# Optimization experiments

Hardware: AMD Instinct MI355X
Metric: run time of the kernel (lower is better)

## Reference

```python
import jax, jax.numpy as jnp
import numpy as np

SEQ_LEN = 512
JOINT_DIM = 96
DECAY = 0.8


def _predefined_weights(n: int, decay: float) -> np.ndarray:
    # W[i, j] = decay**(i-j) for j <= i, each row normalized to sum 1.
    i = np.arange(n)[:, None]
    j = np.arange(n)[None, :]
    lower = j <= i
    exponent = np.where(lower, i - j, 0)
    w = np.where(lower, decay ** exponent.astype(np.float64), 0.0)
    row_sum = w.sum(axis=1, keepdims=True)
    w = np.where(row_sum > 0, w / row_sum, w)
    return w.astype(np.float32)


def setup_inputs() -> dict:
    key = jax.random.key(0)
    kx, ko = jax.random.split(key)
    x = jax.random.normal(kx, (64, SEQ_LEN, JOINT_DIM), dtype=jnp.float32)
    # learnable parameter (initialized to zeros in the module; small noise for generality)
    learnable_offset = 0.02 * jax.random.normal(ko, (JOINT_DIM, SEQ_LEN, SEQ_LEN), dtype=jnp.float32)
    predefined_weights = jnp.asarray(_predefined_weights(SEQ_LEN, DECAY))
    return {"x": x, "learnable_offset": learnable_offset, "predefined_weights": predefined_weights}


def reference(x, learnable_offset, predefined_weights):
    # masks[j] = softmax(predefined + offset[j], axis=-1)   -> [J, N, N]
    masks = jax.nn.softmax(predefined_weights[None, :, :] + learnable_offset, axis=-1)
    # out[b, n, j] = sum_m masks[j, n, m] * x[b, m, j]      -> [B, N, J]
    return jnp.einsum('jnm,bmj->bnj', masks, x)
```

## Files before the change

### kernel.cpp

```cpp
#include <hip/hip_runtime.h>

#define BATCH 64
#define SEQ   512
#define JDIM  96
#define TN    64
#define KC    64
#define NCH   (SEQ / KC)
#define LDB   72

typedef __attribute__((ext_vector_type(8))) short bf16x8;
typedef __attribute__((ext_vector_type(4))) float f32x4;

__device__ __forceinline__ unsigned short f2bf(float f) {
  unsigned u = __float_as_uint(f);
  u += 0x7FFFu + ((u >> 16) & 1u);
  return (unsigned short)(u >> 16);
}

__global__ __launch_bounds__(256) void transpose_in_kernel(
    const float* __restrict__ x, unsigned short* __restrict__ xT) {
  __shared__ float tile[JDIM * 65];
  const int r0 = blockIdx.x * 64;
  const int R = BATCH * SEQ;
  for (int idx = threadIdx.x; idx < 64 * 24; idx += 256) {
    int rr = idx / 24, jg = idx - rr * 24;
    float4 v = *(const float4*)(x + (size_t)(r0 + rr) * JDIM + 4 * jg);
    tile[(4 * jg + 0) * 65 + rr] = v.x;
    tile[(4 * jg + 1) * 65 + rr] = v.y;
    tile[(4 * jg + 2) * 65 + rr] = v.z;
    tile[(4 * jg + 3) * 65 + rr] = v.w;
  }
  __syncthreads();
  for (int idx = threadIdx.x; idx < JDIM * 8; idx += 256) {
    int jj = idx >> 3, rg = idx & 7;
    const float* t = &tile[jj * 65 + 8 * rg];
    uint4 pk;
    pk.x = (unsigned)f2bf(t[0]) | ((unsigned)f2bf(t[1]) << 16);
    pk.y = (unsigned)f2bf(t[2]) | ((unsigned)f2bf(t[3]) << 16);
    pk.z = (unsigned)f2bf(t[4]) | ((unsigned)f2bf(t[5]) << 16);
    pk.w = (unsigned)f2bf(t[6]) | ((unsigned)f2bf(t[7]) << 16);
    *(uint4*)(&xT[(size_t)jj * R + r0 + 8 * rg]) = pk;
  }
}

__global__ __launch_bounds__(256, 3) void fused_kernel(
    const unsigned short* __restrict__ xT,
    const float* __restrict__ off,
    const float* __restrict__ pre,
    float* __restrict__ outT) {
  __shared__ unsigned short As[BATCH * LDB];
  __shared__ unsigned short Bs[TN * LDB];
  __shared__ float Lred[TN * 17];
  __shared__ float Linv[TN];

  const int j  = blockIdx.x % JDIM;
  const int n0 = (blockIdx.x / JDIM) * TN;

  const int tid  = threadIdx.x;
  const int lane = tid & 63;
  const int wid  = tid >> 6;
  const int ln   = lane & 15;
  const int quad = lane >> 4;
  const int bw   = (wid & 1) * 32;
  const int nw   = (wid >> 1) * 32;

  f32x4 acc[2][2];
#pragma unroll
  for (int i = 0; i < 2; ++i)
#pragma unroll
    for (int q = 0; q < 2; ++q) acc[i][q] = (f32x4){0.f, 0.f, 0.f, 0.f};
  float Lpart[4] = {0.f, 0.f, 0.f, 0.f};

  const unsigned short* xTj = xT + (size_t)j * (BATCH * SEQ);
  const float* offj = off + (size_t)j * (SEQ * SEQ);

  const int a_kg = tid & 7;
  const int a_b  = tid >> 3;
  const int b_mg = tid & 15;
  const int b_n  = tid >> 4;

  const unsigned short* pA = xTj + (size_t)a_b * SEQ + 8 * a_kg;
  const float* pO = offj + (size_t)(n0 + b_n) * SEQ + 4 * b_mg;
  const float* pP = pre  + (size_t)(n0 + b_n) * SEQ + 4 * b_mg;

  uint4  rA[2];
  float4 rO[4], rP[4];

  rA[0] = *(const uint4*)(pA);
  rA[1] = *(const uint4*)(pA + 32 * SEQ);
#pragma unroll
  for (int p = 0; p < 4; ++p) {
    rO[p] = *(const float4*)(pO + (size_t)(16 * p) * SEQ);
    rP[p] = *(const float4*)(pP + (size_t)(16 * p) * SEQ);
  }

  for (int ch = 0; ch < NCH; ++ch) {
    *(uint4*)(&As[a_b * LDB + 8 * a_kg]) = rA[0];
    *(uint4*)(&As[(a_b + 32) * LDB + 8 * a_kg]) = rA[1];
#pragma unroll
    for (int p = 0; p < 4; ++p) {
      const float e0 = __expf(rO[p].x + rP[p].x);
      const float e1 = __expf(rO[p].y + rP[p].y);
      const float e2 = __expf(rO[p].z + rP[p].z);
      const float e3 = __expf(rO[p].w + rP[p].w);
      Lpart[p] += (e0 + e1) + (e2 + e3);
      uint2 pk;
      pk.x = (unsigned)f2bf(e0) | ((unsigned)f2bf(e1) << 16);
      pk.y = (unsigned)f2bf(e2) | ((unsigned)f2bf(e3) << 16);
      *(uint2*)(&Bs[(b_n + 16 * p) * LDB + 4 * b_mg]) = pk;
    }
    __syncthreads();

    if (ch + 1 < NCH) {
      const int m1 = (ch + 1) * KC;
      rA[0] = *(const uint4*)(pA + m1);
      rA[1] = *(const uint4*)(pA + 32 * SEQ + m1);
#pragma unroll
      for (int p = 0; p < 4; ++p) {
        rO[p] = *(const float4*)(pO + (size_t)(16 * p) * SEQ + m1);
        rP[p] = *(const float4*)(pP + (size_t)(16 * p) * SEQ + m1);
      }
    }

#pragma unroll
    for (int ks = 0; ks < KC; ks += 32) {
      bf16x8 afrag[2], bfrag[2];
#pragma unroll
      for (int i = 0; i < 2; ++i)
        afrag[i] = *(const bf16x8*)(&As[(bw + 16 * i + ln) * LDB + ks + 8 * quad]);
#pragma unroll
      for (int q = 0; q < 2; ++q)
        bfrag[q] = *(const bf16x8*)(&Bs[(nw + 16 * q + ln) * LDB + ks + 8 * quad]);
#pragma unroll
      for (int i = 0; i < 2; ++i)
#pragma unroll
        for (int q = 0; q < 2; ++q)
          acc[i][q] = __builtin_amdgcn_mfma_f32_16x16x32_bf16(afrag[i], bfrag[q], acc[i][q], 0, 0, 0);
    }
    __syncthreads();
  }

#pragma unroll
  for (int p = 0; p < 4; ++p) Lred[(b_n + 16 * p) * 17 + b_mg] = Lpart[p];
  __syncthreads();
  if (tid < TN) {
    float s = 0.f;
#pragma unroll
    for (int i = 0; i < 16; ++i) s += Lred[tid * 17 + i];
    Linv[tid] = 1.0f / s;
  }
  __syncthreads();

  float* outTj = outT + (size_t)j * (SEQ * BATCH);
#pragma unroll
  for (int q = 0; q < 2; ++q) {
    const int nc = nw + 16 * q + ln;
    const float linv = Linv[nc];
#pragma unroll
    for (int i = 0; i < 2; ++i) {
      float4 v;
      v.x = acc[i][q][0] * linv;
      v.y = acc[i][q][1] * linv;
      v.z = acc[i][q][2] * linv;
      v.w = acc[i][q][3] * linv;
      *(float4*)(&outTj[(size_t)(n0 + nc) * BATCH + bw + 16 * i + 4 * quad]) = v;
    }
  }
}

__global__ __launch_bounds__(256) void transpose_out_kernel(
    const float* __restrict__ outT, float* __restrict__ out) {
  __shared__ float tile[JDIM * 65];
  const int n = blockIdx.x;
  for (int idx = threadIdx.x; idx < JDIM * 16; idx += 256) {
    int jj = idx >> 4, g = idx & 15;
    float4 v = *(const float4*)(outT + ((size_t)jj * SEQ + n) * BATCH + 4 * g);
    float* t = &tile[jj * 65 + 4 * g];
    t[0] = v.x; t[1] = v.y; t[2] = v.z; t[3] = v.w;
  }
  __syncthreads();
  for (int idx = threadIdx.x; idx < BATCH * 24; idx += 256) {
    int b = idx / 24, jg = idx - b * 24;
    float4 w;
    w.x = tile[(4 * jg + 0) * 65 + b];
    w.y = tile[(4 * jg + 1) * 65 + b];
    w.z = tile[(4 * jg + 2) * 65 + b];
    w.w = tile[(4 * jg + 3) * 65 + b];
    *(float4*)(out + ((size_t)b * SEQ + n) * JDIM + 4 * jg) = w;
  }
}

extern "C" void kernel_launch(void* const* d_in, const int* in_sizes, int n_in,
                              void* d_out, int out_size, void* d_ws, size_t ws_size,
                              hipStream_t stream) {
  const float* x   = (const float*)d_in[0];
  const float* off = (const float*)d_in[1];
  const float* pre = (const float*)d_in[2];
  float* out = (float*)d_out;

  unsigned short* xT = (unsigned short*)d_ws;
  float* outT = (float*)((char*)d_ws + (size_t)JDIM * BATCH * SEQ * sizeof(unsigned short));

  transpose_in_kernel<<<BATCH * SEQ / 64, 256, 0, stream>>>(x, xT);
  fused_kernel<<<JDIM * (SEQ / TN), 256, 0, stream>>>(xT, off, pre, outT);
  transpose_out_kernel<<<SEQ, 256, 0, stream>>>(outT, out);
}
```

Measured before the change: 183.7 us.

## Load MFMA fragments directly from global memory, removing LDS staging and barriers

Restructures the fused kernel so each wave owns 16 output rows and loads its offset/predefined values and bf16 x fragments straight from global memory into MFMA operand registers. Shared-memory tiles, the double-buffered register prefetch and all block barriers are gone, and the row-sum reduction now uses two lane shuffles instead of an LDS reduction. In exchange, each wave reloads the full 64-batch x slice for its own rows, so global/L2 traffic for x is four times higher, and there is no explicit software prefetch. The loop is fully unrolled over 512 elements, which may raise register pressure.

```diff
diff --git a/kernel.cpp b/kernel.cpp
--- a/kernel.cpp
+++ b/kernel.cpp
@@ -4,9 +4,6 @@
 #define SEQ   512
 #define JDIM  96
 #define TN    64
-#define KC    64
-#define NCH   (SEQ / KC)
-#define LDB   72
 
 typedef __attribute__((ext_vector_type(8))) short bf16x8;
 typedef __attribute__((ext_vector_type(4))) float f32x4;
@@ -43,16 +40,11 @@
   }
 }
 
-__global__ __launch_bounds__(256, 3) void fused_kernel(
+__global__ __launch_bounds__(256) void fused_kernel(
     const unsigned short* __restrict__ xT,
     const float* __restrict__ off,
     const float* __restrict__ pre,
     float* __restrict__ outT) {
-  __shared__ unsigned short As[BATCH * LDB];
-  __shared__ unsigned short Bs[TN * LDB];
-  __shared__ float Lred[TN * 17];
-  __shared__ float Linv[TN];
-
   const int j  = blockIdx.x % JDIM;
   const int n0 = (blockIdx.x / JDIM) * TN;
 
@@ -61,110 +53,63 @@
   const int wid  = tid >> 6;
   const int ln   = lane & 15;
   const int quad = lane >> 4;
-  const int bw   = (wid & 1) * 32;
-  const int nw   = (wid >> 1) * 32;
-
-  f32x4 acc[2][2];
-#pragma unroll
-  for (int i = 0; i < 2; ++i)
-#pragma unroll
-    for (int q = 0; q < 2; ++q) acc[i][q] = (f32x4){0.f, 0.f, 0.f, 0.f};
-  float Lpart[4] = {0.f, 0.f, 0.f, 0.f};
+  const int nrow = n0 + 16 * wid + ln;
 
   const unsigned short* xTj = xT + (size_t)j * (BATCH * SEQ);
-  const float* offj = off + (size_t)j * (SEQ * SEQ);
+  const float* pO = off + (size_t)j * (SEQ * SEQ) + (size_t)nrow * SEQ + 8 * quad;
+  const float* pP = pre + (size_t)nrow * SEQ + 8 * quad;
+  const unsigned short* pA = xTj + (size_t)ln * SEQ + 8 * quad;
 
-  const int a_kg = tid & 7;
-  const int a_b  = tid >> 3;
-  const int b_mg = tid & 15;
-  const int b_n  = tid >> 4;
+  f32x4 acc[4];
+#pragma unroll
+  for (int i = 0; i < 4; ++i) acc[i] = (f32x4){0.f, 0.f, 0.f, 0.f};
+  float Lsum = 0.f;
 
-  const unsigned short* pA = xTj + (size_t)a_b * SEQ + 8 * a_kg;
-  const float* pO = offj + (size_t)(n0 + b_n) * SEQ + 4 * b_mg;
-  const float* pP = pre  + (size_t)(n0 + b_n) * SEQ + 4 * b_mg;
+#pragma unroll
+  for (int ks = 0; ks < SEQ; ks += 32) {
+    const float4 o0 = *(const float4*)(pO + ks);
+    const float4 o1 = *(const float4*)(pO + ks + 4);
+    const float4 p0 = *(const float4*)(pP + ks);
+    const float4 p1 = *(const float4*)(pP + ks + 4);
+    bf16x8 af[4];
+#pragma unroll
+    for (int i = 0; i < 4; ++i)
+      af[i] = *(const bf16x8*)(pA + (size_t)(16 * i) * SEQ + ks);
 
-  uint4  rA[2];
-  float4 rO[4], rP[4];
+    const float e0 = __expf(o0.x + p0.x);
+    const float e1 = __expf(o0.y + p0.y);
+    const float e2 = __expf(o0.z + p0.z);
+    const float e3 = __expf(o0.w + p0.w);
+    const float e4 = __expf(o1.x + p1.x);
+    const float e5 = __expf(o1.y + p1.y);
+    const float e6 = __expf(o1.z + p1.z);
+    const float e7 = __expf(o1.w + p1.w);
+    Lsum += ((e0 + e1) + (e2 + e3)) + ((e4 + e5) + (e6 + e7));
 
-  rA[0] = *(const uint4*)(pA);
-  rA[1] = *(const uint4*)(pA + 32 * SEQ);
+    union { uint4 u; bf16x8 v; } bp;
+    bp.u.x = (unsigned)f2bf(e0) | ((unsigned)f2bf(e1) << 16);
+    bp.u.y = (unsigned)f2bf(e2) | ((unsigned)f2bf(e3) << 16);
+    bp.u.z = (unsigned)f2bf(e4) | ((unsigned)f2bf(e5) << 16);
+    bp.u.w = (unsigned)f2bf(e6) | ((unsigned)f2bf(e7) << 16);
+
 #pragma unroll
-  for (int p = 0; p < 4; ++p) {
-    rO[p] = *(const float4*)(pO + (size_t)(16 * p) * SEQ);
-    rP[p] = *(const float4*)(pP + (size_t)(16 * p) * SEQ);
+    for (int i = 0; i < 4; ++i)
+      acc[i] = __builtin_amdgcn_mfma_f32_16x16x32_bf16(af[i], bp.v, acc[i], 0, 0, 0);
   }
 
-  for (int ch = 0; ch < NCH; ++ch) {
-    *(uint4*)(&As[a_b * LDB + 8 * a_kg]) = rA[0];
-    *(uint4*)(&As[(a_b + 32) * LDB + 8 * a_kg]) = rA[1];
-#pragma unroll
-    for (int p = 0; p < 4; ++p) {
-      const float e0 = __expf(rO[p].x + rP[p].x);
-      const float e1 = __expf(rO[p].y + rP[p].y);
-      const float e2 = __expf(rO[p].z + rP[p].z);
-      const float e3 = __expf(rO[p].w + rP[p].w);
-      Lpart[p] += (e0 + e1) + (e2 + e3);
-      uint2 pk;
-      pk.x = (unsigned)f2bf(e0) | ((unsigned)f2bf(e1) << 16);
-      pk.y = (unsigned)f2bf(e2) | ((unsigned)f2bf(e3) << 16);
-      *(uint2*)(&Bs[(b_n + 16 * p) * LDB + 4 * b_mg]) = pk;
-    }
-    __syncthreads();
-
-    if (ch + 1 < NCH) {
-      const int m1 = (ch + 1) * KC;
-      rA[0] = *(const uint4*)(pA + m1);
-      rA[1] = *(const uint4*)(pA + 32 * SEQ + m1);
-#pragma unroll
-      for (int p = 0; p < 4; ++p) {
-        rO[p] = *(const float4*)(pO + (size_t)(16 * p) * SEQ + m1);
-        rP[p] = *(const float4*)(pP + (size_t)(16 * p) * SEQ + m1);
-      }
-    }
-
-#pragma unroll
-    for (int ks = 0; ks < KC; ks += 32) {
-      bf16x8 afrag[2], bfrag[2];
-#pragma unroll
-      for (int i = 0; i < 2; ++i)
-        afrag[i] = *(const bf16x8*)(&As[(bw + 16 * i + ln) * LDB + ks + 8 * quad]);
-#pragma unroll
-      for (int q = 0; q < 2; ++q)
-        bfrag[q] = *(const bf16x8*)(&Bs[(nw + 16 * q + ln) * LDB + ks + 8 * quad]);
-#pragma unroll
-      for (int i = 0; i < 2; ++i)
-#pragma unroll
-        for (int q = 0; q < 2; ++q)
-          acc[i][q] = __builtin_amdgcn_mfma_f32_16x16x32_bf16(afrag[i], bfrag[q], acc[i][q], 0, 0, 0);
-    }
-    __syncthreads();
-  }
-
-#pragma unroll
-  for (int p = 0; p < 4; ++p) Lred[(b_n + 16 * p) * 17 + b_mg] = Lpart[p];
-  __syncthreads();
-  if (tid < TN) {
-    float s = 0.f;
-#pragma unroll
-    for (int i = 0; i < 16; ++i) s += Lred[tid * 17 + i];
-    Linv[tid] = 1.0f / s;
-  }
-  __syncthreads();
+  Lsum += __shfl_xor(Lsum, 16, 64);
+  Lsum += __shfl_xor(Lsum, 32, 64);
+  const float linv = 1.0f / Lsum;
 
   float* outTj = outT + (size_t)j * (SEQ * BATCH);
 #pragma unroll
-  for (int q = 0; q < 2; ++q) {
-    const int nc = nw + 16 * q + ln;
-    const float linv = Linv[nc];
-#pragma unroll
-    for (int i = 0; i < 2; ++i) {
-      float4 v;
-      v.x = acc[i][q][0] * linv;
-      v.y = acc[i][q][1] * linv;
-      v.z = acc[i][q][2] * linv;
-      v.w = acc[i][q][3] * linv;
-      *(float4*)(&outTj[(size_t)(n0 + nc) * BATCH + bw + 16 * i + 4 * quad]) = v;
-    }
+  for (int i = 0; i < 4; ++i) {
+    float4 v;
+    v.x = acc[i][0] * linv;
+    v.y = acc[i][1] * linv;
+    v.z = acc[i][2] * linv;
+    v.w = acc[i][3] * linv;
+    *(float4*)(&outTj[(size_t)nrow * BATCH + 16 * i + 4 * quad]) = v;
   }
 }
 
```

After: 189.5 us. +3.1%, slower.

## Split softmax exp into separate kernel producing normalized bf16 masks for GEMM

Applied to the files above, without the earlier changes.

Moves the exp/normalization of predefined+offset into a standalone kernel that writes a normalized bf16 mask tensor, and simplifies the GEMM kernel to load bf16 tiles of xT and the mask directly. This removes per-block exp work and the row-sum reduction from the GEMM, and drops the register prefetch pipelining. In exchange it adds a full write and re-read of a large intermediate mask buffer and changes block-to-work mapping and LDS stride.

```diff
diff --git a/kernel.cpp b/kernel.cpp
--- a/kernel.cpp
+++ b/kernel.cpp
@@ -5,8 +5,7 @@
 #define JDIM  96
 #define TN    64
 #define KC    64
-#define NCH   (SEQ / KC)
-#define LDB   72
+#define LDT   80
 
 typedef __attribute__((ext_vector_type(8))) short bf16x8;
 typedef __attribute__((ext_vector_type(4))) float f32x4;
@@ -43,18 +42,43 @@
   }
 }
 
-__global__ __launch_bounds__(256, 3) void fused_kernel(
+__global__ __launch_bounds__(256) void exp_kernel(
+    const float* __restrict__ off, const float* __restrict__ pre,
+    unsigned short* __restrict__ expoff) {
+  const int row  = (blockIdx.x << 2) + (threadIdx.x >> 6);
+  const int lane = threadIdx.x & 63;
+  const int n    = row & (SEQ - 1);
+  const float* po = off + (size_t)row * SEQ + 8 * lane;
+  const float* pp = pre + (size_t)n * SEQ + 8 * lane;
+  const float4 a0 = *(const float4*)(po);
+  const float4 a1 = *(const float4*)(po + 4);
+  const float4 b0 = *(const float4*)(pp);
+  const float4 b1 = *(const float4*)(pp + 4);
+  const float e0 = __expf(a0.x + b0.x), e1 = __expf(a0.y + b0.y);
+  const float e2 = __expf(a0.z + b0.z), e3 = __expf(a0.w + b0.w);
+  const float e4 = __expf(a1.x + b1.x), e5 = __expf(a1.y + b1.y);
+  const float e6 = __expf(a1.z + b1.z), e7 = __expf(a1.w + b1.w);
+  float s = ((e0 + e1) + (e2 + e3)) + ((e4 + e5) + (e6 + e7));
+#pragma unroll
+  for (int d = 1; d < 64; d <<= 1) s += __shfl_xor(s, d, 64);
+  const float inv = 1.0f / s;
+  uint4 pk;
+  pk.x = (unsigned)f2bf(e0 * inv) | ((unsigned)f2bf(e1 * inv) << 16);
+  pk.y = (unsigned)f2bf(e2 * inv) | ((unsigned)f2bf(e3 * inv) << 16);
+  pk.z = (unsigned)f2bf(e4 * inv) | ((unsigned)f2bf(e5 * inv) << 16);
+  pk.w = (unsigned)f2bf(e6 * inv) | ((unsigned)f2bf(e7 * inv) << 16);
+  *(uint4*)(expoff + (size_t)row * SEQ + 8 * lane) = pk;
+}
+
+__global__ __launch_bounds__(256) void gemm_kernel(
     const unsigned short* __restrict__ xT,
-    const float* __restrict__ off,
-    const float* __restrict__ pre,
+    const unsigned short* __restrict__ expoff,
     float* __restrict__ outT) {
-  __shared__ unsigned short As[BATCH * LDB];
-  __shared__ unsigned short Bs[TN * LDB];
-  __shared__ float Lred[TN * 17];
-  __shared__ float Linv[TN];
+  __shared__ unsigned short As[BATCH * LDT];
+  __shared__ unsigned short Bs[TN * LDT];
 
-  const int j  = blockIdx.x % JDIM;
-  const int n0 = (blockIdx.x / JDIM) * TN;
+  const int j  = blockIdx.x >> 3;
+  const int n0 = (blockIdx.x & 7) * TN;
 
   const int tid  = threadIdx.x;
   const int lane = tid & 63;
@@ -69,68 +93,29 @@
   for (int i = 0; i < 2; ++i)
 #pragma unroll
     for (int q = 0; q < 2; ++q) acc[i][q] = (f32x4){0.f, 0.f, 0.f, 0.f};
-  float Lpart[4] = {0.f, 0.f, 0.f, 0.f};
 
   const unsigned short* xTj = xT + (size_t)j * (BATCH * SEQ);
-  const float* offj = off + (size_t)j * (SEQ * SEQ);
+  const unsigned short* eoj = expoff + (size_t)j * (SEQ * SEQ) + (size_t)n0 * SEQ;
 
-  const int a_kg = tid & 7;
-  const int a_b  = tid >> 3;
-  const int b_mg = tid & 15;
-  const int b_n  = tid >> 4;
+  const int kg = tid & 7;
+  const int rl = tid >> 3;
 
-  const unsigned short* pA = xTj + (size_t)a_b * SEQ + 8 * a_kg;
-  const float* pO = offj + (size_t)(n0 + b_n) * SEQ + 4 * b_mg;
-  const float* pP = pre  + (size_t)(n0 + b_n) * SEQ + 4 * b_mg;
-
-  uint4  rA[2];
-  float4 rO[4], rP[4];
-
-  rA[0] = *(const uint4*)(pA);
-  rA[1] = *(const uint4*)(pA + 32 * SEQ);
-#pragma unroll
-  for (int p = 0; p < 4; ++p) {
-    rO[p] = *(const float4*)(pO + (size_t)(16 * p) * SEQ);
-    rP[p] = *(const float4*)(pP + (size_t)(16 * p) * SEQ);
-  }
-
-  for (int ch = 0; ch < NCH; ++ch) {
-    *(uint4*)(&As[a_b * LDB + 8 * a_kg]) = rA[0];
-    *(uint4*)(&As[(a_b + 32) * LDB + 8 * a_kg]) = rA[1];
-#pragma unroll
-    for (int p = 0; p < 4; ++p) {
-      const float e0 = __expf(rO[p].x + rP[p].x);
-      const float e1 = __expf(rO[p].y + rP[p].y);
-      const float e2 = __expf(rO[p].z + rP[p].z);
-      const float e3 = __expf(rO[p].w + rP[p].w);
-      Lpart[p] += (e0 + e1) + (e2 + e3);
-      uint2 pk;
-      pk.x = (unsigned)f2bf(e0) | ((unsigned)f2bf(e1) << 16);
-      pk.y = (unsigned)f2bf(e2) | ((unsigned)f2bf(e3) << 16);
-      *(uint2*)(&Bs[(b_n + 16 * p) * LDB + 4 * b_mg]) = pk;
-    }
+  for (int ch = 0; ch < SEQ / KC; ++ch) {
+    const int m0 = ch * KC;
+    *(uint4*)(&As[rl * LDT + 8 * kg])        = *(const uint4*)(xTj + (size_t)rl * SEQ + m0 + 8 * kg);
+    *(uint4*)(&As[(rl + 32) * LDT + 8 * kg]) = *(const uint4*)(xTj + (size_t)(rl + 32) * SEQ + m0 + 8 * kg);
+    *(uint4*)(&Bs[rl * LDT + 8 * kg])        = *(const uint4*)(eoj + (size_t)rl * SEQ + m0 + 8 * kg);
+    *(uint4*)(&Bs[(rl + 32) * LDT + 8 * kg]) = *(const uint4*)(eoj + (size_t)(rl + 32) * SEQ + m0 + 8 * kg);
     __syncthreads();
-
-    if (ch + 1 < NCH) {
-      const int m1 = (ch + 1) * KC;
-      rA[0] = *(const uint4*)(pA + m1);
-      rA[1] = *(const uint4*)(pA + 32 * SEQ + m1);
-#pragma unroll
-      for (int p = 0; p < 4; ++p) {
-        rO[p] = *(const float4*)(pO + (size_t)(16 * p) * SEQ + m1);
-        rP[p] = *(const float4*)(pP + (size_t)(16 * p) * SEQ + m1);
-      }
-    }
-
 #pragma unroll
     for (int ks = 0; ks < KC; ks += 32) {
       bf16x8 afrag[2], bfrag[2];
 #pragma unroll
       for (int i = 0; i < 2; ++i)
-        afrag[i] = *(const bf16x8*)(&As[(bw + 16 * i + ln) * LDB + ks + 8 * quad]);
+        afrag[i] = *(const bf16x8*)(&As[(bw + 16 * i + ln) * LDT + ks + 8 * quad]);
 #pragma unroll
       for (int q = 0; q < 2; ++q)
-        bfrag[q] = *(const bf16x8*)(&Bs[(nw + 16 * q + ln) * LDB + ks + 8 * quad]);
+        bfrag[q] = *(const bf16x8*)(&Bs[(nw + 16 * q + ln) * LDT + ks + 8 * quad]);
 #pragma unroll
       for (int i = 0; i < 2; ++i)
 #pragma unroll
@@ -140,29 +125,17 @@
     __syncthreads();
   }
 
-#pragma unroll
-  for (int p = 0; p < 4; ++p) Lred[(b_n + 16 * p) * 17 + b_mg] = Lpart[p];
-  __syncthreads();
-  if (tid < TN) {
-    float s = 0.f;
-#pragma unroll
-    for (int i = 0; i < 16; ++i) s += Lred[tid * 17 + i];
-    Linv[tid] = 1.0f / s;
-  }
-  __syncthreads();
-
   float* outTj = outT + (size_t)j * (SEQ * BATCH);
 #pragma unroll
   for (int q = 0; q < 2; ++q) {
     const int nc = nw + 16 * q + ln;
-    const float linv = Linv[nc];
 #pragma unroll
     for (int i = 0; i < 2; ++i) {
       float4 v;
-      v.x = acc[i][q][0] * linv;
-      v.y = acc[i][q][1] * linv;
-      v.z = acc[i][q][2] * linv;
-      v.w = acc[i][q][3] * linv;
+      v.x = acc[i][q][0];
+      v.y = acc[i][q][1];
+      v.z = acc[i][q][2];
+      v.w = acc[i][q][3];
       *(float4*)(&outTj[(size_t)(n0 + nc) * BATCH + bw + 16 * i + 4 * quad]) = v;
     }
   }
@@ -198,10 +171,13 @@
   const float* pre = (const float*)d_in[2];
   float* out = (float*)d_out;
 
-  unsigned short* xT = (unsigned short*)d_ws;
-  float* outT = (float*)((char*)d_ws + (size_t)JDIM * BATCH * SEQ * sizeof(unsigned short));
+  char* ws = (char*)d_ws;
+  unsigned short* xT     = (unsigned short*)ws;
+  unsigned short* expoff = (unsigned short*)(ws + 6815744);
+  float*          outT   = (float*)(ws + 6815744 + 50331648);
 
   transpose_in_kernel<<<BATCH * SEQ / 64, 256, 0, stream>>>(x, xT);
-  fused_kernel<<<JDIM * (SEQ / TN), 256, 0, stream>>>(xT, off, pre, outT);
+  exp_kernel<<<JDIM * SEQ / 4, 256, 0, stream>>>(off, pre, expoff);
+  gemm_kernel<<<JDIM * (SEQ / TN), 256, 0, stream>>>(xT, expoff, outT);
   transpose_out_kernel<<<SEQ, 256, 0, stream>>>(outT, out);
 }
```

Result: slower. 188.2 us (+2.4%).
